# Kernel optimization log

Measured on AMD Instinct MI355X. Metric: run time of the kernel, lower is better.

Reference implementation:

```python
import jax, jax.numpy as jnp
import numpy as np

N_NODES = 100000
N_EDGES = 1600000
N_GRAPHS = 64
F_IN = 128
HEADS = 4
C = 16
HID = HEADS * C  # 64
N_HIDDEN_LAYERS = 6
NUM_CLASSES = 10
NEG_SLOPE = 0.2


def _gat_layer(h_in, src, dst, W, a_src, a_dst, b):
    # h_in: [N, F]; W: [F, H*C]; a_src/a_dst: [H, C]; b: [H*C]
    N = h_in.shape[0]
    h = (h_in @ W).reshape(N, HEADS, C)                      # [N,H,C]
    alpha_s = jnp.sum(h * a_src, axis=-1)                    # [N,H]
    alpha_d = jnp.sum(h * a_dst, axis=-1)                    # [N,H]
    e = jax.nn.leaky_relu(alpha_s[src] + alpha_d[dst], NEG_SLOPE)  # [E,H]
    # per-destination softmax (self-loops guarantee every node has an in-edge)
    m = jax.ops.segment_max(e, dst, num_segments=N)
    e = jnp.exp(e - m[dst])
    denom = jax.ops.segment_sum(e, dst, num_segments=N)
    w = e / (denom[dst] + 1e-16)                             # [E,H]
    msg = h[src] * w[:, :, None]                             # [E,H,C]
    out = jax.ops.segment_sum(msg, dst, num_segments=N)      # [N,H,C]
    return out.reshape(N, HID) + b


def setup_inputs() -> dict:
    key = jax.random.key(0)
    ks = jax.random.split(key, 16)
    x = jax.random.normal(ks[0], (N_NODES, F_IN), dtype=jnp.float32)
    edge_index = jax.random.randint(ks[1], (2, N_EDGES), 0, N_NODES, dtype=jnp.int64)
    batch = jnp.sort(jax.random.randint(ks[2], (N_NODES,), 0, N_GRAPHS, dtype=jnp.int64))

    def glorot(k, shape):
        fan = shape[0] + shape[-1]
        return jax.random.uniform(k, shape, jnp.float32, -1.0, 1.0) * np.sqrt(6.0 / fan)

    W_in = glorot(ks[3], (F_IN, HID))
    asrc_in = glorot(ks[4], (HEADS, C))
    adst_in = glorot(ks[5], (HEADS, C))
    b_in = jnp.zeros((HID,), jnp.float32)

    W_h = glorot(ks[6], (N_HIDDEN_LAYERS, HID, HID))
    asrc_h = glorot(ks[7], (N_HIDDEN_LAYERS, HEADS, C))
    adst_h = glorot(ks[8], (N_HIDDEN_LAYERS, HEADS, C))
    b_h = jnp.zeros((N_HIDDEN_LAYERS, HID), jnp.float32)

    W1 = glorot(ks[9], (HID, 2 * C))
    b1 = jnp.zeros((2 * C,), jnp.float32)
    W2 = glorot(ks[10], (2 * C, NUM_CLASSES))
    b2 = jnp.zeros((NUM_CLASSES,), jnp.float32)

    return {"x": x, "edge_index": edge_index, "batch": batch,
            "W_in": W_in, "asrc_in": asrc_in, "adst_in": adst_in, "b_in": b_in,
            "W_h": W_h, "asrc_h": asrc_h, "adst_h": adst_h, "b_h": b_h,
            "W1": W1, "b1": b1, "W2": W2, "b2": b2}


def reference(x, edge_index, batch, W_in, asrc_in, adst_in, b_in,
              W_h, asrc_h, adst_h, b_h, W1, b1, W2, b2):
    N = x.shape[0]
    loops = jnp.arange(N, dtype=edge_index.dtype)
    src = jnp.concatenate([edge_index[0], loops])  # add self-loops (PyG default)
    dst = jnp.concatenate([edge_index[1], loops])

    h = jax.nn.relu(_gat_layer(x, src, dst, W_in, asrc_in, adst_in, b_in))
    for i in range(N_HIDDEN_LAYERS):
        h = jax.nn.relu(_gat_layer(h, src, dst, W_h[i], asrc_h[i], adst_h[i], b_h[i]))

    g = jax.ops.segment_max(h, batch, num_segments=N_GRAPHS)  # global_max_pool [G, HID]
    g = jax.nn.relu(g @ W1 + b1)
    return g @ W2 + b2
```

## Files before the change

### kernel.cpp

```cpp
#include <hip/hip_runtime.h>
#include <hip/hip_bf16.h>

#define NN 100000
#define NE 1600000
#define ET 1700000
#define NG 64
#define F_IN 128
#define HID 64
#define NLAYERS 6
#define NEG 0.2f
#define NB_SCAN ((NN + 1023) / 1024)
#define NPART 8
#define PBLK 128
#define PNN (NN / NPART)
#define DCAP 64

typedef __attribute__((ext_vector_type(8))) short bf16x8;
typedef __attribute__((ext_vector_type(4))) float f32x4;

static __device__ __forceinline__ unsigned short f2bf(float f) {
    __hip_bfloat16 b = __float2bfloat16(f);
    return *reinterpret_cast<unsigned short*>(&b);
}
static __device__ __forceinline__ float bf2f(unsigned short u) {
    __hip_bfloat16 b = *reinterpret_cast<__hip_bfloat16*>(&u);
    return __bfloat162float(b);
}

__global__ __launch_bounds__(256) void k_hist(const int* __restrict__ ei,
                                              int* __restrict__ counts) {
    const int part = blockIdx.x & (NPART - 1);
    const int sub  = blockIdx.x >> 3;
    const int lo = part * PNN, hi = lo + PNN;
    for (int e = sub * 256 + threadIdx.x; e < ET; e += PBLK * 256) {
        int dst = (e < NE) ? ei[NE + e] : (e - NE);
        if (dst >= lo && dst < hi) atomicAdd(&counts[dst], 1);
    }
}

__global__ void k_scan_blocks(const int* __restrict__ counts,
                              int* __restrict__ excl, int* __restrict__ bsums) {
    __shared__ int sh[256];
    int b = blockIdx.x, t = threadIdx.x;
    int base = b * 1024 + t * 4;
    int c[4];
    #pragma unroll
    for (int j = 0; j < 4; ++j) {
        int idx = base + j;
        c[j] = (idx < NN) ? counts[idx] : 0;
    }
    int s = c[0] + c[1] + c[2] + c[3];
    sh[t] = s;
    __syncthreads();
    for (int off = 1; off < 256; off <<= 1) {
        int v = (t >= off) ? sh[t - off] : 0;
        __syncthreads();
        sh[t] += v;
        __syncthreads();
    }
    int run = sh[t] - s;
    #pragma unroll
    for (int j = 0; j < 4; ++j) {
        int idx = base + j;
        if (idx < NN) excl[idx] = run;
        run += c[j];
    }
    if (t == 255) bsums[b] = sh[t];
}

__global__ void k_scan_partials(const int* __restrict__ bsums, int* __restrict__ boffs) {
    if (threadIdx.x == 0 && blockIdx.x == 0) {
        int run = 0;
        for (int i = 0; i < NB_SCAN; ++i) { boffs[i] = run; run += bsums[i]; }
    }
}

__global__ void k_add_offsets(int* __restrict__ rowptr, const int* __restrict__ boffs,
                              int* __restrict__ cursor) {
    int idx = blockIdx.x * blockDim.x + threadIdx.x;
    if (idx < NN) {
        int v = rowptr[idx] + boffs[blockIdx.x];
        rowptr[idx] = v;
        cursor[idx] = v;
    }
    if (idx == 0) rowptr[NN] = ET;
}

__global__ __launch_bounds__(256) void k_scatter(const int* __restrict__ ei,
                                                 int* __restrict__ cursor,
                                                 int* __restrict__ csr_src) {
    const int part = blockIdx.x & (NPART - 1);
    const int sub  = blockIdx.x >> 3;
    const int lo = part * PNN, hi = lo + PNN;
    for (int e = sub * 256 + threadIdx.x; e < ET; e += PBLK * 256) {
        int dst = (e < NE) ? ei[NE + e] : (e - NE);
        if (dst >= lo && dst < hi) {
            int src = (e < NE) ? ei[e] : dst;
            int pos = atomicAdd(&cursor[dst], 1);
            csr_src[pos] = src;
        }
    }
}

template<int F, bool BIN>
__global__ __launch_bounds__(256) void k_gemm_alpha(
    const void* __restrict__ hin_,
    const float* __restrict__ W,
    const float* __restrict__ asrc,
    const float* __restrict__ adst,
    unsigned short* __restrict__ hw,
    float* __restrict__ as_,
    float* __restrict__ ad_)
{
    __shared__ float hs[64][36];
    __shared__ float Ws[32][64];
    const int t = threadIdx.x;
    const int n0 = blockIdx.x * 64;
    const int tc = t & 15;
    const int tn = t >> 4;

    float acc[4][4] = {};

    for (int kt = 0; kt < F; kt += 32) {
        __syncthreads();
        #pragma unroll
        for (int u = 0; u < 2; ++u) {
            int idx = t + u * 256;
            int row = idx >> 3, q = idx & 7;
            int gn = n0 + row;
            if constexpr (BIN) {
                const unsigned short* hb = (const unsigned short*)hin_;
                ushort4 uv = (gn < NN)
                    ? *reinterpret_cast<const ushort4*>(&hb[(size_t)gn * F + kt + q * 4])
                    : make_ushort4(0, 0, 0, 0);
                hs[row][q * 4 + 0] = bf2f(uv.x);
                hs[row][q * 4 + 1] = bf2f(uv.y);
                hs[row][q * 4 + 2] = bf2f(uv.z);
                hs[row][q * 4 + 3] = bf2f(uv.w);
            } else {
                const float* hf = (const float*)hin_;
                float4 v = (gn < NN)
                    ? *reinterpret_cast<const float4*>(&hf[(size_t)gn * F + kt + q * 4])
                    : make_float4(0.f, 0.f, 0.f, 0.f);
                hs[row][q * 4 + 0] = v.x;
                hs[row][q * 4 + 1] = v.y;
                hs[row][q * 4 + 2] = v.z;
                hs[row][q * 4 + 3] = v.w;
            }
        }
        #pragma unroll
        for (int u = 0; u < 2; ++u) {
            int idx = t + u * 256;
            int r = idx >> 4, c = idx & 15;
            *reinterpret_cast<float4*>(&Ws[r][c * 4]) =
                *reinterpret_cast<const float4*>(&W[(size_t)(kt + r) * 64 + c * 4]);
        }
        __syncthreads();
        #pragma unroll
        for (int k = 0; k < 32; ++k) {
            const float4 bv = *reinterpret_cast<const float4*>(&Ws[k][tc * 4]);
            float a0 = hs[tn * 4 + 0][k];
            float a1 = hs[tn * 4 + 1][k];
            float a2 = hs[tn * 4 + 2][k];
            float a3 = hs[tn * 4 + 3][k];
            acc[0][0] += a0 * bv.x; acc[0][1] += a0 * bv.y; acc[0][2] += a0 * bv.z; acc[0][3] += a0 * bv.w;
            acc[1][0] += a1 * bv.x; acc[1][1] += a1 * bv.y; acc[1][2] += a1 * bv.z; acc[1][3] += a1 * bv.w;
            acc[2][0] += a2 * bv.x; acc[2][1] += a2 * bv.y; acc[2][2] += a2 * bv.z; acc[2][3] += a2 * bv.w;
            acc[3][0] += a3 * bv.x; acc[3][1] += a3 * bv.y; acc[3][2] += a3 * bv.z; acc[3][3] += a3 * bv.w;
        }
    }

    const int head = tc >> 2;
    #pragma unroll
    for (int i = 0; i < 4; ++i) {
        int n = n0 + tn * 4 + i;
        if (n < NN) {
            ushort4 v;
            v.x = f2bf(acc[i][0]);
            v.y = f2bf(acc[i][1]);
            v.z = f2bf(acc[i][2]);
            v.w = f2bf(acc[i][3]);
            *reinterpret_cast<ushort4*>(&hw[(size_t)n * 64 + tc * 4]) = v;
        }
        float vs = 0.f, vd = 0.f;
        #pragma unroll
        for (int j = 0; j < 4; ++j) {
            int c = (tc * 4 + j) & 15;
            vs += acc[i][j] * asrc[head * 16 + c];
            vd += acc[i][j] * adst[head * 16 + c];
        }
        vs += __shfl_xor(vs, 1); vs += __shfl_xor(vs, 2);
        vd += __shfl_xor(vd, 1); vd += __shfl_xor(vd, 2);
        if ((tc & 3) == 0 && n < NN) {
            as_[n * 4 + head] = vs;
            ad_[n * 4 + head] = vd;
        }
    }
}

__global__ __launch_bounds__(256) void k_gemm_mfma(
    const unsigned short* __restrict__ A,
    const float* __restrict__ W,
    const float* __restrict__ asrc,
    const float* __restrict__ adst,
    unsigned short* __restrict__ hw,
    float* __restrict__ as_,
    float* __restrict__ ad_)
{
    __shared__ unsigned short Wt[64][72];
    const int t = threadIdx.x;
    const int w = t >> 6, lane = t & 63;
    const int n0 = blockIdx.x * 64;

    #pragma unroll
    for (int u = 0; u < 4; ++u) {
        int i = t + u * 256;
        int r = i >> 4, c4 = (i & 15) * 4;
        float4 v = *reinterpret_cast<const float4*>(&W[(size_t)r * 64 + c4]);
        Wt[c4 + 0][r] = f2bf(v.x);
        Wt[c4 + 1][r] = f2bf(v.y);
        Wt[c4 + 2][r] = f2bf(v.z);
        Wt[c4 + 3][r] = f2bf(v.w);
    }
    __syncthreads();

    const int arow = n0 + w * 16 + (lane & 15);
    const int arc = (arow < NN) ? arow : 0;
    const int ak = (lane >> 4) * 8;
    bf16x8 afrag[2];
    #pragma unroll
    for (int kk = 0; kk < 2; ++kk)
        afrag[kk] = *reinterpret_cast<const bf16x8*>(&A[(size_t)arc * 64 + kk * 32 + ak]);

    f32x4 acc[4] = {};
    #pragma unroll
    for (int ct = 0; ct < 4; ++ct) {
        #pragma unroll
        for (int kk = 0; kk < 2; ++kk) {
            bf16x8 bfrag = *reinterpret_cast<const bf16x8*>(&Wt[ct * 16 + (lane & 15)][kk * 32 + ak]);
            acc[ct] = __builtin_amdgcn_mfma_f32_16x16x32_bf16(afrag[kk], bfrag, acc[ct], 0, 0, 0);
        }
    }

    const int c = lane & 15;
    const int r0 = w * 16 + ((lane >> 4) << 2);
    #pragma unroll
    for (int ct = 0; ct < 4; ++ct) {
        const float asv = asrc[ct * 16 + c];
        const float adv = adst[ct * 16 + c];
        #pragma unroll
        for (int reg = 0; reg < 4; ++reg) {
            int node = n0 + r0 + reg;
            float val = acc[ct][reg];
            if (node < NN) hw[(size_t)node * 64 + ct * 16 + c] = f2bf(val);
            float vs = val * asv, vd = val * adv;
            vs += __shfl_xor(vs, 1); vs += __shfl_xor(vs, 2);
            vs += __shfl_xor(vs, 4); vs += __shfl_xor(vs, 8);
            vd += __shfl_xor(vd, 1); vd += __shfl_xor(vd, 2);
            vd += __shfl_xor(vd, 4); vd += __shfl_xor(vd, 8);
            if (c == 0 && node < NN) {
                as_[node * 4 + ct] = vs;
                ad_[node * 4 + ct] = vd;
            }
        }
    }
}

__global__ __launch_bounds__(256) void k_aggregate(
    const unsigned short* __restrict__ hw,
    const float* __restrict__ as_,
    const float* __restrict__ ad_,
    const int* __restrict__ rowptr,
    const int* __restrict__ csr_src,
    const float* __restrict__ bias,
    unsigned short* __restrict__ outA)
{
    __shared__ float pls[4][DCAP][4];
    __shared__ int   sls[4][DCAP];
    const int wv = threadIdx.x >> 6;
    int wave = (blockIdx.x * blockDim.x + threadIdx.x) >> 6;
    int lane = threadIdx.x & 63;
    if (wave >= NN) return;
    const int n = wave;
    const int beg = rowptr[n], end = rowptr[n + 1];
    const int deg = end - beg;
    const int h1 = lane & 3;
    const int sl = lane >> 2;
    const float adn1 = ad_[(unsigned)n * 4u + (unsigned)h1];

    if (deg <= DCAP) {
        float m = -1e30f;
        for (int j = sl; j < deg; j += 16) {
            int s = csr_src[beg + j];
            float e = as_[(unsigned)s * 4u + (unsigned)h1] + adn1;
            e = (e > 0.f) ? e : NEG * e;
            if (h1 == 0) sls[wv][j] = s;
            pls[wv][j][h1] = e;
            m = fmaxf(m, e);
        }
        #pragma unroll
        for (int off = 4; off < 64; off <<= 1)
            m = fmaxf(m, __shfl_xor(m, off));

        float l = 0.f;
        for (int j = sl; j < deg; j += 16) {
            float p = __expf(pls[wv][j][h1] - m);
            pls[wv][j][h1] = p;
            l += p;
        }
        #pragma unroll
        for (int off = 4; off < 64; off <<= 1)
            l += __shfl_xor(l, off);
        const float inv_l = 1.f / (l + 1e-16f);

        const int c16 = lane & 15;
        const int eg  = lane >> 4;
        const int hh  = c16 >> 2;
        const float il2 = __shfl(inv_l, hh);
        float a0 = 0.f, a1 = 0.f, a2 = 0.f, a3 = 0.f;
        for (int i = 0; i < deg; i += 4) {
            int e = i + eg;
            bool act = e < deg;
            int ec = act ? e : 0;
            int s = sls[wv][ec];
            float p = act ? pls[wv][ec][hh] : 0.f;
            ushort4 uv = *reinterpret_cast<const ushort4*>(&hw[((unsigned)s << 6) + (unsigned)(c16 << 2)]);
            a0 += p * bf2f(uv.x);
            a1 += p * bf2f(uv.y);
            a2 += p * bf2f(uv.z);
            a3 += p * bf2f(uv.w);
        }
        a0 += __shfl_xor(a0, 16); a0 += __shfl_xor(a0, 32);
        a1 += __shfl_xor(a1, 16); a1 += __shfl_xor(a1, 32);
        a2 += __shfl_xor(a2, 16); a2 += __shfl_xor(a2, 32);
        a3 += __shfl_xor(a3, 16); a3 += __shfl_xor(a3, 32);
        if (eg == 0) {
            float4 bv = *reinterpret_cast<const float4*>(&bias[c16 * 4]);
            float o0 = a0 * il2 + bv.x;
            float o1 = a1 * il2 + bv.y;
            float o2 = a2 * il2 + bv.z;
            float o3 = a3 * il2 + bv.w;
            ushort4 ov;
            ov.x = f2bf((o0 > 0.f) ? o0 : 0.f);
            ov.y = f2bf((o1 > 0.f) ? o1 : 0.f);
            ov.z = f2bf((o2 > 0.f) ? o2 : 0.f);
            ov.w = f2bf((o3 > 0.f) ? o3 : 0.f);
            *reinterpret_cast<ushort4*>(&outA[((unsigned)n << 6) + (unsigned)(c16 << 2)]) = ov;
        }
    } else {
        const int h2 = lane >> 4;
        float m = -1e30f, l = 0.f;
        for (int j = sl; j < deg; j += 16) {
            int s = csr_src[beg + j];
            float e = as_[(unsigned)s * 4u + (unsigned)h1] + adn1;
            e = (e > 0.f) ? e : NEG * e;
            float mn = fmaxf(m, e);
            l = l * __expf(m - mn) + __expf(e - mn);
            m = mn;
        }
        #pragma unroll
        for (int off = 4; off < 64; off <<= 1) {
            float m2 = __shfl_xor(m, off);
            float l2 = __shfl_xor(l, off);
            float mn = fmaxf(m, m2);
            l = l * __expf(m - mn) + l2 * __expf(m2 - mn);
            m = mn;
        }
        const float inv_l = 1.f / (l + 1e-16f);
        const float mh2 = __shfl(m, h2);
        const float il2 = __shfl(inv_l, h2);
        const float adn2 = ad_[(unsigned)n * 4u + (unsigned)h2];
        float acc = 0.f;
        for (int i = 0; i < deg; ++i) {
            int s = csr_src[beg + i];
            float e = as_[(unsigned)s * 4u + (unsigned)h2] + adn2;
            e = (e > 0.f) ? e : NEG * e;
            acc += __expf(e - mh2) * bf2f(hw[((unsigned)s << 6) | (unsigned)lane]);
        }
        float o = acc * il2 + bias[lane];
        outA[((unsigned)n << 6) | (unsigned)lane] = f2bf((o > 0.f) ? o : 0.f);
    }
}

__global__ void k_pool(const unsigned short* __restrict__ h, const int* __restrict__ batch,
                       unsigned int* __restrict__ g) {
    int wave = (blockIdx.x * blockDim.x + threadIdx.x) >> 6;
    int lane = threadIdx.x & 63;
    int n0 = wave * 32;
    if (n0 >= NN) return;
    int n1 = n0 + 32; if (n1 > NN) n1 = NN;
    int cg = batch[n0];
    float m = 0.f;
    for (int n = n0; n < n1; ++n) {
        int gi = batch[n];
        if (gi != cg) {
            atomicMax(&g[cg * 64 + lane], __float_as_uint(m));
            m = 0.f; cg = gi;
        }
        m = fmaxf(m, bf2f(h[((unsigned)n << 6) | (unsigned)lane]));
    }
    atomicMax(&g[cg * 64 + lane], __float_as_uint(m));
}

__global__ void k_head(const unsigned int* __restrict__ gbits,
                       const float* __restrict__ W1, const float* __restrict__ b1,
                       const float* __restrict__ W2, const float* __restrict__ b2,
                       float* __restrict__ out) {
    __shared__ float gs[NG * 64];
    __shared__ float z1[NG * 32];
    int t = threadIdx.x;
    for (int i = t; i < NG * 64; i += 256) gs[i] = __uint_as_float(gbits[i]);
    __syncthreads();
    for (int i = t; i < NG * 32; i += 256) {
        int gi = i >> 5, c = i & 31;
        float acc = b1[c];
        for (int k = 0; k < 64; ++k) acc += gs[gi * 64 + k] * W1[k * 32 + c];
        z1[i] = (acc > 0.f) ? acc : 0.f;
    }
    __syncthreads();
    for (int i = t; i < NG * 10; i += 256) {
        int gi = i / 10, c = i % 10;
        float acc = b2[c];
        for (int k = 0; k < 32; ++k) acc += z1[gi * 32 + k] * W2[k * 10 + c];
        out[i] = acc;
    }
}

extern "C" void kernel_launch(void* const* d_in, const int* in_sizes, int n_in,
                              void* d_out, int out_size, void* d_ws, size_t ws_size,
                              hipStream_t stream) {
    const float* x       = (const float*)d_in[0];
    const int*   ei      = (const int*)d_in[1];
    const int*   batch   = (const int*)d_in[2];
    const float* W_in    = (const float*)d_in[3];
    const float* asrc_in = (const float*)d_in[4];
    const float* adst_in = (const float*)d_in[5];
    const float* b_in    = (const float*)d_in[6];
    const float* W_hid   = (const float*)d_in[7];
    const float* asrc_h  = (const float*)d_in[8];
    const float* adst_h  = (const float*)d_in[9];
    const float* b_hid   = (const float*)d_in[10];
    const float* W1      = (const float*)d_in[11];
    const float* b1      = (const float*)d_in[12];
    const float* W2      = (const float*)d_in[13];
    const float* b2      = (const float*)d_in[14];
    float* out = (float*)d_out;

    char* base = (char*)d_ws;
    size_t off = 0;
    auto alloc = [&](size_t bytes) -> char* {
        char* p = base + off;
        off += (bytes + 255) & ~size_t(255);
        return p;
    };
    unsigned short* A  = (unsigned short*)alloc((size_t)NN * 64 * 2);
    unsigned short* Bf = (unsigned short*)alloc((size_t)NN * 64 * 2);
    float* as_    = (float*)alloc((size_t)NN * 4 * 4);
    float* ad_    = (float*)alloc((size_t)NN * 4 * 4);
    int*   counts = (int*)alloc((size_t)NN * 4);
    int*   rowptr = (int*)alloc((size_t)(NN + 1) * 4);
    int*   cursor = (int*)alloc((size_t)(NN + 1) * 4);
    int*   bsums  = (int*)alloc((size_t)NB_SCAN * 4);
    int*   boffs  = (int*)alloc((size_t)NB_SCAN * 4);
    int*   csr    = (int*)alloc((size_t)ET * 4);
    unsigned int* g = (unsigned int*)alloc((size_t)NG * 64 * 4);

    hipMemsetAsync(counts, 0, (size_t)NN * 4, stream);
    hipMemsetAsync(g, 0, (size_t)NG * 64 * 4, stream);

    k_hist<<<NPART * PBLK, 256, 0, stream>>>(ei, counts);
    k_scan_blocks<<<NB_SCAN, 256, 0, stream>>>(counts, rowptr, bsums);
    k_scan_partials<<<1, 64, 0, stream>>>(bsums, boffs);
    k_add_offsets<<<NB_SCAN, 1024, 0, stream>>>(rowptr, boffs, cursor);
    k_scatter<<<NPART * PBLK, 256, 0, stream>>>(ei, cursor, csr);

    const int gemm_blocks = (NN + 63) / 64;
    const int node_blocks = (NN * 64 + 255) / 256;

    k_gemm_alpha<128, false><<<gemm_blocks, 256, 0, stream>>>(x, W_in, asrc_in, adst_in, Bf, as_, ad_);
    k_aggregate<<<node_blocks, 256, 0, stream>>>(Bf, as_, ad_, rowptr, csr, b_in, A);

    for (int i = 0; i < NLAYERS; ++i) {
        k_gemm_mfma<<<gemm_blocks, 256, 0, stream>>>(
            A, W_hid + (size_t)i * 64 * 64, asrc_h + (size_t)i * 64, adst_h + (size_t)i * 64,
            Bf, as_, ad_);
        k_aggregate<<<node_blocks, 256, 0, stream>>>(Bf, as_, ad_, rowptr, csr, b_hid + (size_t)i * 64, A);
    }

    int pool_waves = (NN + 31) / 32;
    int pool_blocks = (pool_waves * 64 + 255) / 256;
    k_pool<<<pool_blocks, 256, 0, stream>>>(A, batch, g);
    k_head<<<1, 256, 0, stream>>>(g, W1, b1, W2, b2, out);
}
```

Measured before the change: 786.7 us.

## Split attention-logit computation out of MFMA GEMM and unroll CSR build loops

Removes the per-element shuffle reductions for the attention logits from the hidden-layer MFMA GEMM and computes them in a separate k_alpha kernel that re-reads the bf16 features, one thread per node-head. The CSR histogram and scatter kernels get twice as many blocks and a 4-way unrolled loop that issues edge loads before the atomics. The aim is to shorten the GEMM epilogue and raise memory-level parallelism in the CSR build. In exchange each layer costs an extra launch and an extra pass over the features, and the logits are now computed from bf16-rounded values rather than fp32 accumulators.

```diff
diff --git a/kernel.cpp b/kernel.cpp
--- a/kernel.cpp
+++ b/kernel.cpp
@@ -11,7 +11,7 @@
 #define NEG 0.2f
 #define NB_SCAN ((NN + 1023) / 1024)
 #define NPART 8
-#define PBLK 128
+#define PBLK 256
 #define PNN (NN / NPART)
 #define DCAP 64
 
@@ -32,9 +32,17 @@
     const int part = blockIdx.x & (NPART - 1);
     const int sub  = blockIdx.x >> 3;
     const int lo = part * PNN, hi = lo + PNN;
-    for (int e = sub * 256 + threadIdx.x; e < ET; e += PBLK * 256) {
-        int dst = (e < NE) ? ei[NE + e] : (e - NE);
-        if (dst >= lo && dst < hi) atomicAdd(&counts[dst], 1);
+    const int S = PBLK * 256;
+    for (int e0 = sub * 256 + threadIdx.x; e0 < ET; e0 += 4 * S) {
+        int e[4], d[4];
+        #pragma unroll
+        for (int u = 0; u < 4; ++u) {
+            e[u] = e0 + u * S;
+            d[u] = (e[u] < ET) ? ((e[u] < NE) ? ei[NE + e[u]] : (e[u] - NE)) : -1;
+        }
+        #pragma unroll
+        for (int u = 0; u < 4; ++u)
+            if (d[u] >= lo && d[u] < hi) atomicAdd(&counts[d[u]], 1);
     }
 }
 
@@ -92,12 +100,21 @@
     const int part = blockIdx.x & (NPART - 1);
     const int sub  = blockIdx.x >> 3;
     const int lo = part * PNN, hi = lo + PNN;
-    for (int e = sub * 256 + threadIdx.x; e < ET; e += PBLK * 256) {
-        int dst = (e < NE) ? ei[NE + e] : (e - NE);
-        if (dst >= lo && dst < hi) {
-            int src = (e < NE) ? ei[e] : dst;
-            int pos = atomicAdd(&cursor[dst], 1);
-            csr_src[pos] = src;
+    const int S = PBLK * 256;
+    for (int e0 = sub * 256 + threadIdx.x; e0 < ET; e0 += 4 * S) {
+        int e[4], d[4];
+        #pragma unroll
+        for (int u = 0; u < 4; ++u) {
+            e[u] = e0 + u * S;
+            d[u] = (e[u] < ET) ? ((e[u] < NE) ? ei[NE + e[u]] : (e[u] - NE)) : -1;
+        }
+        #pragma unroll
+        for (int u = 0; u < 4; ++u) {
+            if (d[u] >= lo && d[u] < hi) {
+                int src = (e[u] < NE) ? ei[e[u]] : d[u];
+                int pos = atomicAdd(&cursor[d[u]], 1);
+                csr_src[pos] = src;
+            }
         }
     }
 }
@@ -201,11 +218,7 @@
 __global__ __launch_bounds__(256) void k_gemm_mfma(
     const unsigned short* __restrict__ A,
     const float* __restrict__ W,
-    const float* __restrict__ asrc,
-    const float* __restrict__ adst,
-    unsigned short* __restrict__ hw,
-    float* __restrict__ as_,
-    float* __restrict__ ad_)
+    unsigned short* __restrict__ hw)
 {
     __shared__ unsigned short Wt[64][72];
     const int t = threadIdx.x;
@@ -246,24 +259,41 @@
     const int r0 = w * 16 + ((lane >> 4) << 2);
     #pragma unroll
     for (int ct = 0; ct < 4; ++ct) {
-        const float asv = asrc[ct * 16 + c];
-        const float adv = adst[ct * 16 + c];
         #pragma unroll
         for (int reg = 0; reg < 4; ++reg) {
             int node = n0 + r0 + reg;
-            float val = acc[ct][reg];
-            if (node < NN) hw[(size_t)node * 64 + ct * 16 + c] = f2bf(val);
-            float vs = val * asv, vd = val * adv;
-            vs += __shfl_xor(vs, 1); vs += __shfl_xor(vs, 2);
-            vs += __shfl_xor(vs, 4); vs += __shfl_xor(vs, 8);
-            vd += __shfl_xor(vd, 1); vd += __shfl_xor(vd, 2);
-            vd += __shfl_xor(vd, 4); vd += __shfl_xor(vd, 8);
-            if (c == 0 && node < NN) {
-                as_[node * 4 + ct] = vs;
-                ad_[node * 4 + ct] = vd;
-            }
-        }
-    }
+            if (node < NN) hw[(size_t)node * 64 + ct * 16 + c] = f2bf(acc[ct][reg]);
+        }
+    }
+}
+
+__global__ __launch_bounds__(256) void k_alpha(
+    const unsigned short* __restrict__ hw,
+    const float* __restrict__ asrc,
+    const float* __restrict__ adst,
+    float* __restrict__ as_,
+    float* __restrict__ ad_)
+{
+    int t = blockIdx.x * 256 + threadIdx.x;
+    if (t >= NN * 4) return;
+    int h = t & 3;
+    const bf16x8* row = reinterpret_cast<const bf16x8*>(&hw[((unsigned)(t >> 2) << 6) + (unsigned)(h << 4)]);
+    bf16x8 v0 = row[0], v1 = row[1];
+    float vs = 0.f, vd = 0.f;
+    #pragma unroll
+    for (int j = 0; j < 8; ++j) {
+        float f = bf2f((unsigned short)v0[j]);
+        vs += f * asrc[h * 16 + j];
+        vd += f * adst[h * 16 + j];
+    }
+    #pragma unroll
+    for (int j = 0; j < 8; ++j) {
+        float f = bf2f((unsigned short)v1[j]);
+        vs += f * asrc[h * 16 + 8 + j];
+        vd += f * adst[h * 16 + 8 + j];
+    }
+    as_[t] = vs;
+    ad_[t] = vd;
 }
 
 __global__ __launch_bounds__(256) void k_aggregate(
@@ -476,14 +506,14 @@
 
     const int gemm_blocks = (NN + 63) / 64;
     const int node_blocks = (NN * 64 + 255) / 256;
+    const int alpha_blocks = (NN * 4 + 255) / 256;
 
     k_gemm_alpha<128, false><<<gemm_blocks, 256, 0, stream>>>(x, W_in, asrc_in, adst_in, Bf, as_, ad_);
     k_aggregate<<<node_blocks, 256, 0, stream>>>(Bf, as_, ad_, rowptr, csr, b_in, A);
 
     for (int i = 0; i < NLAYERS; ++i) {
-        k_gemm_mfma<<<gemm_blocks, 256, 0, stream>>>(
-            A, W_hid + (size_t)i * 64 * 64, asrc_h + (size_t)i * 64, adst_h + (size_t)i * 64,
-            Bf, as_, ad_);
+        k_gemm_mfma<<<gemm_blocks, 256, 0, stream>>>(A, W_hid + (size_t)i * 64 * 64, Bf);
+        k_alpha<<<alpha_blocks, 256, 0, stream>>>(Bf, asrc_h + (size_t)i * 64, adst_h + (size_t)i * 64, as_, ad_);
         k_aggregate<<<node_blocks, 256, 0, stream>>>(Bf, as_, ad_, rowptr, csr, b_hid + (size_t)i * 64, A);
     }
 
```

After: 762.6 us. 3.1% less time.
